# Kernel tuning notes

Measured on AMD Instinct MI355X. Metric: run time of the kernel, lower is better.

## Reference

```python
import jax, jax.numpy as jnp
import numpy as np

N, E, B, D = 50000, 800000, 250, 128
EPS = 1e-5


def setup_inputs() -> dict:
    key = jax.random.key(0)
    ks = jax.random.split(key, 12)
    x = jax.random.normal(ks[0], (N, D), jnp.float32)
    w = jax.random.uniform(ks[1], (E, 4), jnp.float32)
    src = jax.random.randint(ks[2], (E,), 0, N)
    dst = jax.random.randint(ks[3], (E,), 0, N)
    graph_ids = jnp.sort(jax.random.randint(ks[4], (N,), 0, B))
    s = 1.0 / np.sqrt(D)
    W1 = jax.random.normal(ks[5], (D, D), jnp.float32) * s
    W2 = jax.random.normal(ks[6], (D, D), jnp.float32) * s
    W3 = jax.random.normal(ks[7], (D, D), jnp.float32) * s
    ln1_g = jnp.ones((D,), jnp.float32)
    ln1_b = jnp.zeros((D,), jnp.float32)
    ln2_g = jnp.ones((D,), jnp.float32)
    ln2_b = jnp.zeros((D,), jnp.float32)
    return dict(x=x, w=w, W1=W1, W2=W2, W3=W3, ln1_g=ln1_g, ln1_b=ln1_b,
                ln2_g=ln2_g, ln2_b=ln2_b, src=src, dst=dst, graph_ids=graph_ids)


def _layernorm(h, g, b):
    mu = jnp.mean(h, axis=-1, keepdims=True)
    var = jnp.mean(jnp.square(h - mu), axis=-1, keepdims=True)
    return (h - mu) * jax.lax.rsqrt(var + EPS) * g + b


def reference(x, w, W1, W2, W3, ln1_g, ln1_b, ln2_g, ln2_b, src, dst, graph_ids):
    # edge feature [E,Fe] -> scalar edge weight [E] (mean over feature dim)
    w_s = jnp.mean(w, axis=-1)
    ones_e = jnp.ones((E,), x.dtype)
    # DGL norm='both': unweighted degrees, clamped to >= 1
    out_deg = jnp.clip(jax.ops.segment_sum(ones_e, src, num_segments=N), 1.0)
    in_deg = jnp.clip(jax.ops.segment_sum(ones_e, dst, num_segments=N), 1.0)
    out_norm = jax.lax.rsqrt(out_deg)[:, None]  # [N,1]
    in_norm = jax.lax.rsqrt(in_deg)[:, None]    # [N,1]

    def gconv(h, W):
        m = (h * out_norm)[src] * w_s[:, None]                 # [E,D] gather-mul
        agg = jax.ops.segment_sum(m, dst, num_segments=N)      # [N,D] scatter-add
        return (agg * in_norm) @ W                              # [N,D_out]

    h = _layernorm(jax.nn.relu(gconv(x, W1)), ln1_g, ln1_b)
    h = _layernorm(jax.nn.relu(gconv(h, W2)), ln2_g, ln2_b)
    h = gconv(h, W3)
    # per-graph segmented sum readout -> [B, D]
    return jax.ops.segment_sum(h, graph_ids, num_segments=B)
```

## Files before the change

kernel.cpp:

```cpp
#include <hip/hip_runtime.h>

#define D 128
#define RS 16
#define NBMAX 1024
constexpr float EPS = 1e-5f;

typedef short bf16x8 __attribute__((ext_vector_type(8)));
typedef float f32x4 __attribute__((ext_vector_type(4)));

__device__ __forceinline__ uint f2bf(float f) {
  union { float f; uint u; } v; v.f = f;
  return (v.u + 0x7fffu + ((v.u >> 16) & 1u)) >> 16;
}
__device__ __forceinline__ float bflo(uint u) {
  union { uint u; float f; } v; v.u = u << 16; return v.f;
}
__device__ __forceinline__ float bfhi(uint u) {
  union { uint u; float f; } v; v.u = u & 0xffff0000u; return v.f;
}

__device__ __forceinline__ int lower_bound(const int* __restrict__ a, int n, int key) {
  int lo = 0, hi = n;
  while (lo < hi) { int m = (lo + hi) >> 1; if (a[m] < key) lo = m + 1; else hi = m; }
  return lo;
}

__global__ __launch_bounds__(256) void k_pre(
    const int* __restrict__ src, const int* __restrict__ dst,
    int* __restrict__ ocnt, int* __restrict__ btot, int E, int nb, int ebA,
    const float4* __restrict__ x, uint4* __restrict__ xb, int n8, int cb,
    const float* __restrict__ W1, const float* __restrict__ W2,
    const float* __restrict__ W3, ushort* __restrict__ Wf) {
  __shared__ int hloc[NBMAX];
  int bid = blockIdx.x;
  int tid = threadIdx.x;
  if (bid < ebA) {
    for (int j = tid; j < nb; j += 256) hloc[j] = 0;
    __syncthreads();
    int e0 = bid * 4096;
#pragma unroll 4
    for (int it = 0; it < 16; ++it) {
      int e = e0 + it * 256 + tid;
      if (e < E) {
        atomicAdd(&ocnt[src[e]], 1);
        atomicAdd(&hloc[dst[e] >> 6], 1);
      }
    }
    __syncthreads();
    for (int j = tid; j < nb; j += 256) {
      int c = hloc[j];
      if (c) atomicAdd(&btot[j], c);
    }
  } else if (bid < ebA + cb) {
    int i = (bid - ebA) * 256 + tid;
    if (i < n8) {
      float4 p = x[i * 2], q = x[i * 2 + 1];
      uint4 o;
      o.x = f2bf(p.x) | (f2bf(p.y) << 16);
      o.y = f2bf(p.z) | (f2bf(p.w) << 16);
      o.z = f2bf(q.x) | (f2bf(q.y) << 16);
      o.w = f2bf(q.z) | (f2bf(q.w) << 16);
      xb[i] = o;
    }
  } else {
    int t4 = (bid - ebA - cb) * 256 + tid;
    if (t4 < 3 * 2048) {
      const float* Wsrc = (t4 < 2048) ? W1 : (t4 < 4096) ? W2 : W3;
      int t = t4 & 2047;
      int lane = t & 63;
      int frag = t >> 6;
      int ks = frag >> 3, ct = frag & 7;
      int col = ct * 16 + (lane & 15);
      int kb = ks * 32 + (lane >> 4) * 8;
      uint p[8];
#pragma unroll
      for (int j = 0; j < 8; ++j) p[j] = f2bf(Wsrc[(kb + j) * D + col]);
      uint4 o;
      o.x = p[0] | (p[1] << 16);
      o.y = p[2] | (p[3] << 16);
      o.z = p[4] | (p[5] << 16);
      o.w = p[6] | (p[7] << 16);
      *(uint4*)(Wf + (size_t)t4 * 8) = o;
    }
  }
}

__global__ void k_onorm(const int* __restrict__ ocnt, float* __restrict__ outn, int N) {
  int n = blockIdx.x * 256 + threadIdx.x;
  if (n < N) outn[n] = rsqrtf(fmaxf((float)ocnt[n], 1.0f));
}

__global__ __launch_bounds__(1024) void k_bbase(const int* __restrict__ btot,
                                                int* __restrict__ bb,
                                                int* __restrict__ rowptr,
                                                int nb, int E, int N) {
  __shared__ int part[1024];
  int t = threadIdx.x;
  int v = (t < nb) ? btot[t] : 0;
  part[t] = v;
  __syncthreads();
  for (int off = 1; off < 1024; off <<= 1) {
    int u = (t >= off) ? part[t - off] : 0;
    __syncthreads();
    part[t] += u;
    __syncthreads();
  }
  if (t < nb) bb[t] = part[t] - v;
  if (t == 0) { bb[nb] = E; rowptr[N] = E; }
}

__global__ __launch_bounds__(256) void k_bscatter(
    const int* __restrict__ src, const int* __restrict__ dst,
    const float4* __restrict__ w, const float* __restrict__ outn,
    const int* __restrict__ bb, int* __restrict__ bcur,
    unsigned long long* __restrict__ ebuf, int E, int nb) {
  __shared__ int hloc[NBMAX];
  __shared__ int hcur[NBMAX];
  int bid = blockIdx.x, tid = threadIdx.x;
  for (int j = tid; j < nb; j += 256) hloc[j] = 0;
  __syncthreads();
  int e0 = bid * 4096;
#pragma unroll 4
  for (int it = 0; it < 16; ++it) {
    int e = e0 + it * 256 + tid;
    if (e < E) atomicAdd(&hloc[dst[e] >> 6], 1);
  }
  __syncthreads();
  for (int j = tid; j < nb; j += 256) {
    int c = hloc[j];
    hcur[j] = c ? (bb[j] + atomicAdd(&bcur[j], c)) : 0;
  }
  __syncthreads();
#pragma unroll 4
  for (int it = 0; it < 16; ++it) {
    int e = e0 + it * 256 + tid;
    if (e < E) {
      int d = dst[e], s = src[e];
      int pos = atomicAdd(&hcur[d >> 6], 1);
      float4 wv = w[e];
      float coef = (wv.x + wv.y + wv.z + wv.w) * 0.25f * outn[s];
      unsigned long long pk = ((unsigned long long)__float_as_uint(coef) << 32) |
                              ((unsigned long long)(d & 63) << 16) | (uint)s;
      ebuf[pos] = pk;
    }
  }
}

__global__ __launch_bounds__(256) void k_bplace(
    const unsigned long long* __restrict__ ebuf, const int* __restrict__ bb,
    int* __restrict__ rowptr, float* __restrict__ innm,
    int* __restrict__ src_p, float* __restrict__ coef_p, int N) {
  __shared__ int c64[64], ex[64], cur[64];
  int b = blockIdx.x, tid = threadIdx.x;
  int base = bb[b];
  int cnt = bb[b + 1] - base;
  if (tid < 64) c64[tid] = 0;
  __syncthreads();
  for (int i = tid; i < cnt; i += 256) {
    unsigned long long v = ebuf[base + i];
    atomicAdd(&c64[(int)((v >> 16) & 63)], 1);
  }
  __syncthreads();
  if (tid < 64) {
    int cv = c64[tid];
    int inc = cv;
#pragma unroll
    for (int off = 1; off < 64; off <<= 1) {
      int u = __shfl_up(inc, off);
      if (tid >= off) inc += u;
    }
    int excl = inc - cv;
    ex[tid] = excl;
    cur[tid] = 0;
    int node = b * 64 + tid;
    if (node < N) {
      rowptr[node] = base + excl;
      innm[node] = rsqrtf(fmaxf((float)cv, 1.0f));
    }
  }
  __syncthreads();
  for (int i = tid; i < cnt; i += 256) {
    unsigned long long v = ebuf[base + i];
    int dl = (int)((v >> 16) & 63);
    int pos = base + ex[dl] + atomicAdd(&cur[dl], 1);
    src_p[pos] = (int)(v & 0xFFFFu);
    coef_p[pos] = __uint_as_float((uint)(v >> 32));
  }
}

__global__ __launch_bounds__(256) void k_fused(
    const ushort* __restrict__ h, const int* __restrict__ rowptr,
    const int* __restrict__ src_p, const float* __restrict__ coef_p,
    const float* __restrict__ innm, const ushort* __restrict__ Wf,
    const float* __restrict__ g, const float* __restrict__ bta,
    void* __restrict__ out, int N, int do_ln) {
  __shared__ float lds[4][16 * D];
  const int lane = threadIdx.x & 63;
  const int wv = threadIdx.x >> 6;
  const int row0 = blockIdx.x * 64 + wv * 16;
  if (row0 >= N) return;

  ushort* at = (ushort*)&lds[wv][0];
  {
    const int grp = lane >> 4;
    const int c = lane & 15;
    for (int rr = 0; rr < 4; ++rr) {
      int n = row0 + grp * 4 + rr;
      if (n >= N) break;
      int beg = rowptr[n], end = rowptr[n + 1];
      float a0 = 0, a1 = 0, a2 = 0, a3 = 0, a4 = 0, a5 = 0, a6 = 0, a7 = 0;
#define ACC8(q, f)                                          \
  a0 = fmaf(bflo(q.x), f, a0); a1 = fmaf(bfhi(q.x), f, a1); \
  a2 = fmaf(bflo(q.y), f, a2); a3 = fmaf(bfhi(q.y), f, a3); \
  a4 = fmaf(bflo(q.z), f, a4); a5 = fmaf(bfhi(q.z), f, a5); \
  a6 = fmaf(bflo(q.w), f, a6); a7 = fmaf(bfhi(q.w), f, a7);
      int j = beg;
      for (; j + 4 <= end; j += 4) {
        int s0 = src_p[j], s1 = src_p[j + 1], s2 = src_p[j + 2], s3 = src_p[j + 3];
        float f0 = coef_p[j], f1 = coef_p[j + 1], f2 = coef_p[j + 2], f3 = coef_p[j + 3];
        uint4 q0 = *(const uint4*)(h + (size_t)s0 * D + c * 8);
        uint4 q1 = *(const uint4*)(h + (size_t)s1 * D + c * 8);
        uint4 q2 = *(const uint4*)(h + (size_t)s2 * D + c * 8);
        uint4 q3 = *(const uint4*)(h + (size_t)s3 * D + c * 8);
        ACC8(q0, f0) ACC8(q1, f1) ACC8(q2, f2) ACC8(q3, f3)
      }
      for (; j < end; ++j) {
        int s = src_p[j];
        float f = coef_p[j];
        uint4 q = *(const uint4*)(h + (size_t)s * D + c * 8);
        ACC8(q, f)
      }
#undef ACC8
      float sc = innm[n];
      uint4 o;
      o.x = f2bf(a0 * sc) | (f2bf(a1 * sc) << 16);
      o.y = f2bf(a2 * sc) | (f2bf(a3 * sc) << 16);
      o.z = f2bf(a4 * sc) | (f2bf(a5 * sc) << 16);
      o.w = f2bf(a6 * sc) | (f2bf(a7 * sc) << 16);
      *(uint4*)(at + (grp * 4 + rr) * 136 + c * 8) = o;
    }
  }
  asm volatile("s_waitcnt lgkmcnt(0)" ::: "memory");
  __builtin_amdgcn_sched_barrier(0);

  const int lc = lane & 15, lg = lane >> 4;
  f32x4 acc[8];
#pragma unroll
  for (int ct = 0; ct < 8; ++ct) acc[ct] = (f32x4){0.f, 0.f, 0.f, 0.f};
#pragma unroll
  for (int ks = 0; ks < 4; ++ks) {
    bf16x8 a = *(const bf16x8*)(at + lc * 136 + ks * 32 + lg * 8);
    const ushort* wp = Wf + ((size_t)(ks * 8) * 64 + lane) * 8;
#pragma unroll
    for (int ct = 0; ct < 8; ++ct) {
      bf16x8 b = *(const bf16x8*)(wp + ct * 512);
      acc[ct] = __builtin_amdgcn_mfma_f32_16x16x32_bf16(a, b, acc[ct], 0, 0, 0);
    }
  }
  asm volatile("s_waitcnt lgkmcnt(0)" ::: "memory");
  __builtin_amdgcn_sched_barrier(0);

  if (do_ln) {
    float v[8][4];
#pragma unroll
    for (int ct = 0; ct < 8; ++ct)
#pragma unroll
      for (int j = 0; j < 4; ++j) v[ct][j] = fmaxf(acc[ct][j], 0.f);
    float mu[4], rs[4];
#pragma unroll
    for (int j = 0; j < 4; ++j) {
      float s = 0.f;
#pragma unroll
      for (int ct = 0; ct < 8; ++ct) s += v[ct][j];
#pragma unroll
      for (int off = 1; off < 16; off <<= 1) s += __shfl_xor(s, off);
      mu[j] = s * (1.0f / D);
    }
#pragma unroll
    for (int j = 0; j < 4; ++j) {
      float q = 0.f;
#pragma unroll
      for (int ct = 0; ct < 8; ++ct) {
        v[ct][j] -= mu[j];
        q = fmaf(v[ct][j], v[ct][j], q);
      }
#pragma unroll
      for (int off = 1; off < 16; off <<= 1) q += __shfl_xor(q, off);
      rs[j] = rsqrtf(q * (1.0f / D) + EPS);
    }
    ushort* lp = (ushort*)&lds[wv][0];
#pragma unroll
    for (int ct = 0; ct < 8; ++ct) {
      float gc = g[ct * 16 + lc], bc = bta[ct * 16 + lc];
#pragma unroll
      for (int j = 0; j < 4; ++j)
        lp[(lg * 4 + j) * D + ct * 16 + lc] = (ushort)f2bf(fmaf(v[ct][j] * rs[j], gc, bc));
    }
    __builtin_amdgcn_wave_barrier();
    int r = row0 + (lane >> 2);
    if (r < N) {
      ushort* ob = (ushort*)out + (size_t)row0 * D + lane * 32;
#pragma unroll
      for (int i = 0; i < 4; ++i)
        ((uint4*)ob)[i] = ((const uint4*)(lp + lane * 32))[i];
    }
  } else {
    float* lp = &lds[wv][0];
#pragma unroll
    for (int ct = 0; ct < 8; ++ct)
#pragma unroll
      for (int j = 0; j < 4; ++j)
        lp[(lg * 4 + j) * D + ct * 16 + lc] = acc[ct][j];
    __builtin_amdgcn_wave_barrier();
    int r = row0 + (lane >> 2);
    if (r < N) {
      float* ob = (float*)out + (size_t)row0 * D + lane * 32;
#pragma unroll
      for (int i = 0; i < 8; ++i)
        ((float4*)ob)[i] = ((const float4*)(lp + lane * 32))[i];
    }
  }
}

__global__ __launch_bounds__(128) void k_rpart(
    const float* __restrict__ h, const int* __restrict__ gid,
    float* __restrict__ part, int N) {
  int b = blockIdx.x / RS, s = blockIdx.x % RS;
  int t = threadIdx.x;
  int start = lower_bound(gid, N, b);
  int end = lower_bound(gid, N, b + 1);
  int len = end - start;
  int chunk = (len + RS - 1) / RS;
  int rb = start + s * chunk;
  int re = min(rb + chunk, end);
  float acc = 0.f;
  for (int n = rb; n < re; ++n) acc += h[(size_t)n * D + t];
  part[((size_t)b * RS + s) * D + t] = acc;
}

__global__ __launch_bounds__(128) void k_rsum(
    const float* __restrict__ part, float* __restrict__ out) {
  int b = blockIdx.x;
  int t = threadIdx.x;
  float acc = 0.f;
#pragma unroll
  for (int s = 0; s < RS; ++s) acc += part[((size_t)b * RS + s) * D + t];
  out[(size_t)b * D + t] = acc;
}

extern "C" void kernel_launch(void* const* d_in, const int* in_sizes, int n_in,
                              void* d_out, int out_size, void* d_ws, size_t ws_size,
                              hipStream_t stream) {
  const float* x    = (const float*)d_in[0];
  const float* w    = (const float*)d_in[1];
  const float* W1   = (const float*)d_in[2];
  const float* W2   = (const float*)d_in[3];
  const float* W3   = (const float*)d_in[4];
  const float* ln1g = (const float*)d_in[5];
  const float* ln1b = (const float*)d_in[6];
  const float* ln2g = (const float*)d_in[7];
  const float* ln2b = (const float*)d_in[8];
  const int* src = (const int*)d_in[9];
  const int* dst = (const int*)d_in[10];
  const int* gid = (const int*)d_in[11];
  const int N = in_sizes[0] / D;
  const int E = in_sizes[9];
  const int B = out_size / D;
  float* outp = (float*)d_out;

  float*  h3f  = (float*)d_ws;
  ushort* xb   = (ushort*)(h3f + (size_t)N * D);
  ushort* hb1  = xb + (size_t)N * D;
  ushort* Wf   = hb1 + (size_t)N * D;
  float*  outn = (float*)(Wf + 3 * 2048 * 8);
  float*  innm = outn + N;
  const int nb  = (N + 63) >> 6;
  const int ebA = (E + 4095) / 4096;
  int*    ocnt = (int*)(innm + N);
  int*    btot = ocnt + N;
  int*    bcur = btot + nb;
  int*    rowptr = bcur + nb;
  int*    src_p  = rowptr + N + 1;
  float*  coef_p = (float*)(src_p + E);
  int*    bb   = (int*)(coef_p + E);
  float*  part = (float*)(bb + nb + 1);
  unsigned long long* ebuf = (unsigned long long*)h3f;

  const int mb  = (N + 63) / 64;
  const int n8  = N * D / 8;
  const int cb  = (n8 + 255) / 256;

  hipMemsetAsync(ocnt, 0, sizeof(int) * ((size_t)N + 2 * nb), stream);
  k_pre<<<ebA + cb + 24, 256, 0, stream>>>(src, dst, ocnt, btot, E, nb, ebA,
                                           (const float4*)x, (uint4*)xb, n8, cb,
                                           W1, W2, W3, Wf);
  k_onorm<<<(N + 255) / 256, 256, 0, stream>>>(ocnt, outn, N);
  k_bbase<<<1, 1024, 0, stream>>>(btot, bb, rowptr, nb, E, N);
  k_bscatter<<<ebA, 256, 0, stream>>>(src, dst, (const float4*)w, outn, bb, bcur,
                                      ebuf, E, nb);
  k_bplace<<<nb, 256, 0, stream>>>(ebuf, bb, rowptr, innm, src_p, coef_p, N);

  k_fused<<<mb, 256, 0, stream>>>(xb, rowptr, src_p, coef_p, innm, Wf,
                                  ln1g, ln1b, hb1, N, 1);
  k_fused<<<mb, 256, 0, stream>>>(hb1, rowptr, src_p, coef_p, innm, Wf + 16384,
                                  ln2g, ln2b, xb, N, 1);
  k_fused<<<mb, 256, 0, stream>>>(xb, rowptr, src_p, coef_p, innm, Wf + 32768,
                                  nullptr, nullptr, h3f, N, 0);

  k_rpart<<<B * RS, 128, 0, stream>>>(h3f, gid, part, N);
  k_rsum<<<B, 128, 0, stream>>>(part, outp);
}
```

Baseline: 224.8 us.

## Pack CSR edges as 64-bit and gather directly into MFMA A-operand registers

Source index and coefficient are merged into one 64-bit CSR entry, so each edge costs a single load instead of two. The fused kernel shrinks to one wave per block covering 16 rows. Each lane now owns one row and a k-slice, so the gathered aggregate lands directly in the MFMA A-operand layout and the LDS round-trip for A is skipped. The trade-off is one edge per iteration with no 4-way unroll, plus load imbalance across lanes, since each lane walks its own row's edge list and the wave waits on the longest row.

After: 236.4 us. 1.05x slower.

```diff
diff --git a/kernel.cpp b/kernel.cpp
--- a/kernel.cpp
+++ b/kernel.cpp
@@ -149,7 +149,7 @@
 __global__ __launch_bounds__(256) void k_bplace(
     const unsigned long long* __restrict__ ebuf, const int* __restrict__ bb,
     int* __restrict__ rowptr, float* __restrict__ innm,
-    int* __restrict__ src_p, float* __restrict__ coef_p, int N) {
+    unsigned long long* __restrict__ ecsr, int N) {
   __shared__ int c64[64], ex[64], cur[64];
   int b = blockIdx.x, tid = threadIdx.x;
   int base = bb[b];
@@ -183,82 +183,72 @@
     unsigned long long v = ebuf[base + i];
     int dl = (int)((v >> 16) & 63);
     int pos = base + ex[dl] + atomicAdd(&cur[dl], 1);
-    src_p[pos] = (int)(v & 0xFFFFu);
-    coef_p[pos] = __uint_as_float((uint)(v >> 32));
-  }
-}
-
-__global__ __launch_bounds__(256) void k_fused(
+    ecsr[pos] = (v & 0xFFFFFFFF00000000ull) | (v & 0xFFFFull);
+  }
+}
+
+__global__ __launch_bounds__(64) void k_fused(
     const ushort* __restrict__ h, const int* __restrict__ rowptr,
-    const int* __restrict__ src_p, const float* __restrict__ coef_p,
+    const unsigned long long* __restrict__ ecsr,
     const float* __restrict__ innm, const ushort* __restrict__ Wf,
     const float* __restrict__ g, const float* __restrict__ bta,
     void* __restrict__ out, int N, int do_ln) {
-  __shared__ float lds[4][16 * D];
-  const int lane = threadIdx.x & 63;
-  const int wv = threadIdx.x >> 6;
-  const int row0 = blockIdx.x * 64 + wv * 16;
-  if (row0 >= N) return;
-
-  ushort* at = (ushort*)&lds[wv][0];
-  {
-    const int grp = lane >> 4;
-    const int c = lane & 15;
-    for (int rr = 0; rr < 4; ++rr) {
-      int n = row0 + grp * 4 + rr;
-      if (n >= N) break;
-      int beg = rowptr[n], end = rowptr[n + 1];
-      float a0 = 0, a1 = 0, a2 = 0, a3 = 0, a4 = 0, a5 = 0, a6 = 0, a7 = 0;
-#define ACC8(q, f)                                          \
-  a0 = fmaf(bflo(q.x), f, a0); a1 = fmaf(bfhi(q.x), f, a1); \
-  a2 = fmaf(bflo(q.y), f, a2); a3 = fmaf(bfhi(q.y), f, a3); \
-  a4 = fmaf(bflo(q.z), f, a4); a5 = fmaf(bfhi(q.z), f, a5); \
-  a6 = fmaf(bflo(q.w), f, a6); a7 = fmaf(bfhi(q.w), f, a7);
-      int j = beg;
-      for (; j + 4 <= end; j += 4) {
-        int s0 = src_p[j], s1 = src_p[j + 1], s2 = src_p[j + 2], s3 = src_p[j + 3];
-        float f0 = coef_p[j], f1 = coef_p[j + 1], f2 = coef_p[j + 2], f3 = coef_p[j + 3];
-        uint4 q0 = *(const uint4*)(h + (size_t)s0 * D + c * 8);
-        uint4 q1 = *(const uint4*)(h + (size_t)s1 * D + c * 8);
-        uint4 q2 = *(const uint4*)(h + (size_t)s2 * D + c * 8);
-        uint4 q3 = *(const uint4*)(h + (size_t)s3 * D + c * 8);
-        ACC8(q0, f0) ACC8(q1, f1) ACC8(q2, f2) ACC8(q3, f3)
-      }
-      for (; j < end; ++j) {
-        int s = src_p[j];
-        float f = coef_p[j];
-        uint4 q = *(const uint4*)(h + (size_t)s * D + c * 8);
-        ACC8(q, f)
-      }
+  __shared__ float lds[16 * D];
+  const int lane = threadIdx.x;
+  const int lr = lane & 15, lg = lane >> 4;
+  const int row0 = blockIdx.x * 16;
+  const int row = row0 + lr;
+  const bool valid = row < N;
+
+  int beg = 0, end = 0;
+  float sc = 0.f;
+  if (valid) { beg = rowptr[row]; end = rowptr[row + 1]; sc = innm[row]; }
+
+  float a0[8], a1[8], a2[8], a3[8];
+#pragma unroll
+  for (int i = 0; i < 8; ++i) { a0[i] = 0; a1[i] = 0; a2[i] = 0; a3[i] = 0; }
+
+#define ACC8(A, q, f)                                          \
+  A[0] = fmaf(bflo(q.x), f, A[0]); A[1] = fmaf(bfhi(q.x), f, A[1]); \
+  A[2] = fmaf(bflo(q.y), f, A[2]); A[3] = fmaf(bfhi(q.y), f, A[3]); \
+  A[4] = fmaf(bflo(q.z), f, A[4]); A[5] = fmaf(bfhi(q.z), f, A[5]); \
+  A[6] = fmaf(bflo(q.w), f, A[6]); A[7] = fmaf(bfhi(q.w), f, A[7]);
+  for (int j = beg; j < end; ++j) {
+    unsigned long long v = ecsr[j];
+    float cf = __uint_as_float((uint)(v >> 32));
+    int s = (int)(v & 0xFFFFFFFFu);
+    const ushort* hp = h + (size_t)s * D + lg * 8;
+    uint4 q0 = *(const uint4*)(hp);
+    uint4 q1 = *(const uint4*)(hp + 32);
+    uint4 q2 = *(const uint4*)(hp + 64);
+    uint4 q3 = *(const uint4*)(hp + 96);
+    ACC8(a0, q0, cf) ACC8(a1, q1, cf) ACC8(a2, q2, cf) ACC8(a3, q3, cf)
+  }
 #undef ACC8
-      float sc = innm[n];
-      uint4 o;
-      o.x = f2bf(a0 * sc) | (f2bf(a1 * sc) << 16);
-      o.y = f2bf(a2 * sc) | (f2bf(a3 * sc) << 16);
-      o.z = f2bf(a4 * sc) | (f2bf(a5 * sc) << 16);
-      o.w = f2bf(a6 * sc) | (f2bf(a7 * sc) << 16);
-      *(uint4*)(at + (grp * 4 + rr) * 136 + c * 8) = o;
-    }
-  }
-  asm volatile("s_waitcnt lgkmcnt(0)" ::: "memory");
-  __builtin_amdgcn_sched_barrier(0);
-
-  const int lc = lane & 15, lg = lane >> 4;
+
+  uint4 fa[4];
+#define PACK(dst, A)                                             \
+  dst.x = f2bf(A[0] * sc) | (f2bf(A[1] * sc) << 16);             \
+  dst.y = f2bf(A[2] * sc) | (f2bf(A[3] * sc) << 16);             \
+  dst.z = f2bf(A[4] * sc) | (f2bf(A[5] * sc) << 16);             \
+  dst.w = f2bf(A[6] * sc) | (f2bf(A[7] * sc) << 16);
+  PACK(fa[0], a0) PACK(fa[1], a1) PACK(fa[2], a2) PACK(fa[3], a3)
+#undef PACK
+
   f32x4 acc[8];
 #pragma unroll
   for (int ct = 0; ct < 8; ++ct) acc[ct] = (f32x4){0.f, 0.f, 0.f, 0.f};
 #pragma unroll
   for (int ks = 0; ks < 4; ++ks) {
-    bf16x8 a = *(const bf16x8*)(at + lc * 136 + ks * 32 + lg * 8);
+    bf16x8 av;
+    __builtin_memcpy(&av, &fa[ks], 16);
     const ushort* wp = Wf + ((size_t)(ks * 8) * 64 + lane) * 8;
 #pragma unroll
     for (int ct = 0; ct < 8; ++ct) {
       bf16x8 b = *(const bf16x8*)(wp + ct * 512);
-      acc[ct] = __builtin_amdgcn_mfma_f32_16x16x32_bf16(a, b, acc[ct], 0, 0, 0);
-    }
-  }
-  asm volatile("s_waitcnt lgkmcnt(0)" ::: "memory");
-  __builtin_amdgcn_sched_barrier(0);
+      acc[ct] = __builtin_amdgcn_mfma_f32_16x16x32_bf16(av, b, acc[ct], 0, 0, 0);
+    }
+  }
 
   if (do_ln) {
     float v[8][4];
@@ -288,13 +278,13 @@
       for (int off = 1; off < 16; off <<= 1) q += __shfl_xor(q, off);
       rs[j] = rsqrtf(q * (1.0f / D) + EPS);
     }
-    ushort* lp = (ushort*)&lds[wv][0];
+    ushort* lp = (ushort*)&lds[0];
 #pragma unroll
     for (int ct = 0; ct < 8; ++ct) {
-      float gc = g[ct * 16 + lc], bc = bta[ct * 16 + lc];
+      float gc = g[ct * 16 + lr], bc = bta[ct * 16 + lr];
 #pragma unroll
       for (int j = 0; j < 4; ++j)
-        lp[(lg * 4 + j) * D + ct * 16 + lc] = (ushort)f2bf(fmaf(v[ct][j] * rs[j], gc, bc));
+        lp[(lg * 4 + j) * D + ct * 16 + lr] = (ushort)f2bf(fmaf(v[ct][j] * rs[j], gc, bc));
     }
     __builtin_amdgcn_wave_barrier();
     int r = row0 + (lane >> 2);
@@ -305,12 +295,12 @@
         ((uint4*)ob)[i] = ((const uint4*)(lp + lane * 32))[i];
     }
   } else {
-    float* lp = &lds[wv][0];
+    float* lp = &lds[0];
 #pragma unroll
     for (int ct = 0; ct < 8; ++ct)
 #pragma unroll
       for (int j = 0; j < 4; ++j)
-        lp[(lg * 4 + j) * D + ct * 16 + lc] = acc[ct][j];
+        lp[(lg * 4 + j) * D + ct * 16 + lr] = acc[ct][j];
     __builtin_amdgcn_wave_barrier();
     int r = row0 + (lane >> 2);
     if (r < N) {
@@ -380,13 +370,12 @@
   int*    btot = ocnt + N;
   int*    bcur = btot + nb;
   int*    rowptr = bcur + nb;
-  int*    src_p  = rowptr + N + 1;
-  float*  coef_p = (float*)(src_p + E);
-  int*    bb   = (int*)(coef_p + E);
-  float*  part = (float*)(bb + nb + 1);
+  int*    bb   = rowptr + N + 2;
+  unsigned long long* ecsr = (unsigned long long*)(bb + nb + 2);
+  float*  part = (float*)(ecsr + E);
   unsigned long long* ebuf = (unsigned long long*)h3f;
 
-  const int mb  = (N + 63) / 64;
+  const int mb  = (N + 15) / 16;
   const int n8  = N * D / 8;
   const int cb  = (n8 + 255) / 256;
 
@@ -398,14 +387,14 @@
   k_bbase<<<1, 1024, 0, stream>>>(btot, bb, rowptr, nb, E, N);
   k_bscatter<<<ebA, 256, 0, stream>>>(src, dst, (const float4*)w, outn, bb, bcur,
                                       ebuf, E, nb);
-  k_bplace<<<nb, 256, 0, stream>>>(ebuf, bb, rowptr, innm, src_p, coef_p, N);
-
-  k_fused<<<mb, 256, 0, stream>>>(xb, rowptr, src_p, coef_p, innm, Wf,
-                                  ln1g, ln1b, hb1, N, 1);
-  k_fused<<<mb, 256, 0, stream>>>(hb1, rowptr, src_p, coef_p, innm, Wf + 16384,
-                                  ln2g, ln2b, xb, N, 1);
-  k_fused<<<mb, 256, 0, stream>>>(xb, rowptr, src_p, coef_p, innm, Wf + 32768,
-                                  nullptr, nullptr, h3f, N, 0);
+  k_bplace<<<nb, 256, 0, stream>>>(ebuf, bb, rowptr, innm, ecsr, N);
+
+  k_fused<<<mb, 64, 0, stream>>>(xb, rowptr, ecsr, innm, Wf,
+                                 ln1g, ln1b, hb1, N, 1);
+  k_fused<<<mb, 64, 0, stream>>>(hb1, rowptr, ecsr, innm, Wf + 16384,
+                                 ln2g, ln2b, xb, N, 1);
+  k_fused<<<mb, 64, 0, stream>>>(xb, rowptr, ecsr, innm, Wf + 32768,
+                                 nullptr, nullptr, h3f, N, 0);
 
   k_rpart<<<B * RS, 128, 0, stream>>>(h3f, gid, part, N);
   k_rsum<<<B, 128, 0, stream>>>(part, outp);
```
